# Optimization experiments

Measured on AMD Instinct MI355X. Metric: run time of the kernel, lower is better.

Reference implementation:

```python
import jax, jax.numpy as jnp
import numpy as np

N_NODES = 100000


def _gcn_conv(x, W, b, row, col, norm, n_nodes):
    # PyG GCNConv: h = x @ W; out[i] = sum_{(j->i)} norm_e * h[j] + b
    h = x @ W
    msg = h[row] * norm[:, None]              # [E_tot, out_dim] gather
    out = jax.ops.segment_sum(msg, col, num_segments=n_nodes)  # scatter-add
    return out + b


def _norm_and_loops(edge_index, n_nodes):
    # add self loops, compute symmetric normalization deg^-1/2 * deg^-1/2
    loop = jnp.arange(n_nodes, dtype=edge_index.dtype)
    row = jnp.concatenate([edge_index[0], loop])
    col = jnp.concatenate([edge_index[1], loop])
    deg = jax.ops.segment_sum(jnp.ones_like(col, dtype=jnp.float32), col,
                              num_segments=n_nodes)
    dis = jnp.where(deg > 0, jax.lax.rsqrt(jnp.maximum(deg, 1.0)), 0.0)
    norm = dis[row] * dis[col]
    return row, col, norm


def setup_inputs() -> dict:
    key = jax.random.key(0)
    ks = jax.random.split(key, 9)
    in_c, hid, lat = 128, 128, 64
    n_edges = 1600000
    x = jax.random.normal(ks[0], (N_NODES, in_c), dtype=jnp.float32)
    edge_index = jax.random.randint(ks[1], (2, n_edges), 0, N_NODES, dtype=jnp.int64)
    s1 = 1.0 / np.sqrt(in_c)
    s2 = 1.0 / np.sqrt(hid)
    W1 = jax.random.uniform(ks[2], (in_c, hid), jnp.float32, -s1, s1)
    b1 = jnp.zeros((hid,), jnp.float32)
    W_mu = jax.random.uniform(ks[3], (hid, lat), jnp.float32, -s2, s2)
    b_mu = jnp.zeros((lat,), jnp.float32)
    W_lv = jax.random.uniform(ks[4], (hid, lat), jnp.float32, -s2, s2)
    b_lv = jnp.zeros((lat,), jnp.float32)
    eps = jax.random.normal(ks[5], (N_NODES, lat), dtype=jnp.float32)
    return {"x": x, "edge_index": edge_index, "W1": W1, "b1": b1,
            "W_mu": W_mu, "b_mu": b_mu, "W_lv": W_lv, "b_lv": b_lv,
            "eps": eps}


def reference(x, edge_index, W1, b1, W_mu, b_mu, W_lv, b_lv, eps):
    row, col, norm = _norm_and_loops(edge_index, N_NODES)
    h = jax.nn.relu(_gcn_conv(x, W1, b1, row, col, norm, N_NODES))
    mu = _gcn_conv(h, W_mu, b_mu, row, col, norm, N_NODES)
    logvar = _gcn_conv(h, W_lv, b_lv, row, col, norm, N_NODES)
    # reparameterize (training mode): z = mu + eps * exp(0.5*logvar)
    z = mu + eps * jnp.exp(0.5 * logvar)
    return (z, mu, logvar)
```

## Files before the change

### kernel.cpp

```cpp
#include <hip/hip_runtime.h>
#include <math.h>


#define SHIFT 9
#define EPB 2048
#define BSTRIDE 12288
#define CAP 15104

using f32x4 = __attribute__((ext_vector_type(4))) float;
using f32x2 = __attribute__((ext_vector_type(2))) float;
using f16x8 = __attribute__((ext_vector_type(8))) _Float16;
using f16x2 = __attribute__((ext_vector_type(2))) _Float16;

__device__ inline int scan256(int v, int* wsum) {
    __syncthreads();
    int lane = threadIdx.x & 63, wid = threadIdx.x >> 6;
    int s = v;
#pragma unroll
    for (int d = 1; d < 64; d <<= 1) {
        int u = __shfl_up(s, d, 64);
        if (lane >= d) s += u;
    }
    if (lane == 63) wsum[wid] = s;
    __syncthreads();
    int off = 0;
    for (int w = 0; w < wid; w++) off += wsum[w];
    return off + s - v;
}

__global__ __launch_bounds__(256) void k_bucket(const int* __restrict__ rowi,
                                                const int* __restrict__ coli,
                                                int* __restrict__ bcur,
                                                int* __restrict__ recs,
                                                int E, int NB) {
    __shared__ int lh[4][256], lcur[4][256], excl[256], gbase[256], wsum[4];
    __shared__ int2 stage[EPB];
    int t = threadIdx.x, w = t >> 6;
    lh[0][t] = 0; lh[1][t] = 0; lh[2][t] = 0; lh[3][t] = 0;
    __syncthreads();
    int base = blockIdx.x * EPB;
    int nE = min(EPB, E - base);
    for (int i = t; i < nE; i += 256)
        atomicAdd(&lh[w][coli[base + i] >> SHIFT], 1);
    __syncthreads();
    int h0 = lh[0][t], h1 = lh[1][t], h2 = lh[2][t], h3 = lh[3][t];
    int tot = h0 + h1 + h2 + h3;
    int ex = scan256(tot, wsum);
    excl[t] = ex;
    lcur[0][t] = ex;
    lcur[1][t] = ex + h0;
    lcur[2][t] = ex + h0 + h1;
    lcur[3][t] = ex + h0 + h1 + h2;
    if (t < NB && tot)
        gbase[t] = t * BSTRIDE + atomicAdd(&bcur[t], tot);
    __syncthreads();
    for (int i = t; i < nE; i += 256) {
        int r = rowi[base + i], c = coli[base + i];
        int p = atomicAdd(&lcur[w][c >> SHIFT], 1);
        stage[p] = make_int2(r, c);
    }
    __syncthreads();
    for (int i = t; i < nE; i += 256) {
        int2 r = stage[i];
        int bb = r.y >> SHIFT;
        int idx = gbase[bb] + (i - excl[bb]);
        if (idx - bb * BSTRIDE < BSTRIDE)
            recs[idx] = (r.x << SHIFT) | (r.y & 511);
    }
}

__global__ __launch_bounds__(256) void k_fill2(const int* __restrict__ recs,
                                               const int* __restrict__ bcur,
                                               int2* __restrict__ rowse,
                                               float* __restrict__ dis,
                                               int* __restrict__ srcs, int N) {
    __shared__ int hist[512], excl[512], wsum[4];
    __shared__ int srcsL[CAP];
    int t = threadIdx.x;
    int b = blockIdx.x;
    int nbase = b << SHIFT;
    int start = b * BSTRIDE;
    int cnt = min(bcur[b], BSTRIDE);
    int end = start + cnt;
    hist[t] = 0;
    hist[t + 256] = 0;
    __syncthreads();
    for (int i = start + t; i < end; i += 256)
        atomicAdd(&hist[recs[i] & 511], 1);
    __syncthreads();
    int h0 = hist[2 * t], h1 = hist[2 * t + 1];
    int e0 = scan256(h0 + h1, wsum);
    excl[2 * t] = e0;
    excl[2 * t + 1] = e0 + h0;
    int n0 = nbase + 2 * t, n1 = nbase + 2 * t + 1;
    if (n0 < N) {
        rowse[n0] = make_int2(start + e0, start + e0 + h0);
        dis[n0] = rsqrtf((float)(h0 + 1));
    }
    if (n1 < N) {
        rowse[n1] = make_int2(start + e0 + h0, start + e0 + h0 + h1);
        dis[n1] = rsqrtf((float)(h1 + 1));
    }
    __syncthreads();
    if (cnt <= CAP) {
        for (int i = start + t; i < end; i += 256) {
            int r = recs[i];
            int p = atomicAdd(&excl[r & 511], 1);
            srcsL[p] = ((unsigned)r) >> SHIFT;
        }
        __syncthreads();
        for (int i = t; i < cnt; i += 256) srcs[start + i] = srcsL[i];
    } else {
        for (int i = start + t; i < end; i += 256) {
            int r = recs[i];
            int p = atomicAdd(&excl[r & 511], 1);
            srcs[start + p] = ((unsigned)r) >> SHIFT;
        }
    }
}

template <bool XF16>
__global__ __launch_bounds__(256) void k_gemm(const void* __restrict__ Xv,
                                              const float* __restrict__ Wa,
                                              const float* __restrict__ Wb,
                                              int split,
                                              _Float16* __restrict__ Y,
                                              int M, int ngroups,
                                              int* __restrict__ zcur, int nz) {
    __shared__ _Float16 Wl[16384];
    int tid = threadIdx.x;
    if (zcur && blockIdx.x == 0 && tid < nz) zcur[tid] = 0;
    int wbs = 128 - split;
    for (int i = tid; i < 16384; i += 256) {
        int k = i >> 7, n = i & 127;
        float v = (n < split) ? Wa[k * split + n] : Wb[k * wbs + (n - split)];
        int tt = n >> 4, c = (k >> 5), q = (k >> 3) & 3, ln = q * 16 + (n & 15);
        Wl[(((tt * 4 + c) * 64) + ln) * 8 + (k & 7)] = (_Float16)v;
    }
    __syncthreads();

    int lane = tid & 63, w = tid >> 6;
    f16x8 B[32];
#pragma unroll
    for (int i = 0; i < 32; i++)
        B[i] = *(const f16x8*)&Wl[(i * 64 + lane) * 8];

    int m16 = lane & 15, quad = lane >> 4;
    for (int g = blockIdx.x; g < ngroups; g += gridDim.x) {
        int rowbase = g * 64 + w * 16;
        if (rowbase >= M) continue;
        int arow = min(rowbase + m16, M - 1);
        f16x8 A[4];
        if (XF16) {
            const _Float16* X = (const _Float16*)Xv;
#pragma unroll
            for (int c = 0; c < 4; c++)
                A[c] = *(const f16x8*)&X[arow * 128 + c * 32 + quad * 8];
        } else {
            const float* X = (const float*)Xv;
#pragma unroll
            for (int c = 0; c < 4; c++) {
                float4 u0 = *(const float4*)&X[arow * 128 + c * 32 + quad * 8];
                float4 u1 = *(const float4*)&X[arow * 128 + c * 32 + quad * 8 + 4];
                f16x8 a;
                a[0] = (_Float16)u0.x; a[1] = (_Float16)u0.y;
                a[2] = (_Float16)u0.z; a[3] = (_Float16)u0.w;
                a[4] = (_Float16)u1.x; a[5] = (_Float16)u1.y;
                a[6] = (_Float16)u1.z; a[7] = (_Float16)u1.w;
                A[c] = a;
            }
        }

        f32x4 acc[8];
#pragma unroll
        for (int t = 0; t < 8; t++) acc[t] = (f32x4)(0.f);
#pragma unroll
        for (int t = 0; t < 8; t++)
#pragma unroll
            for (int c = 0; c < 4; c++)
                acc[t] = __builtin_amdgcn_mfma_f32_16x16x32_f16(
                    A[c], B[t * 4 + c], acc[t], 0, 0, 0);

#pragma unroll
        for (int r = 0; r < 4; r++) {
            int row = rowbase + quad * 4 + r;
            if (row < M) {
#pragma unroll
                for (int t = 0; t < 8; t++)
                    Y[row * 128 + t * 16 + m16] = (_Float16)acc[t][r];
            }
        }
    }
}

template <bool OF16>
__global__ __launch_bounds__(256) void k_agg(const _Float16* __restrict__ F,
                                             const float* __restrict__ dis,
                                             const int2* __restrict__ rowse,
                                             const int* __restrict__ srcs,
                                             const float* __restrict__ ba,
                                             const float* __restrict__ bb,
                                             void* __restrict__ outA,
                                             void* __restrict__ outB,
                                             const float* __restrict__ eps,
                                             float* __restrict__ z, int N) {
    int node = blockIdx.x * 4 + (threadIdx.x >> 6);
    if (node >= N) return;
    int lane = threadIdx.x & 63;
    int g = lane >> 4, sl = lane & 15;
    const f16x8* Fr = (const f16x8*)F;

    float di = dis[node];
    float acc[8];
#pragma unroll
    for (int j = 0; j < 8; j++) acc[j] = 0.f;
    if (g == 0) {
        f16x8 v = Fr[node * 16 + sl];
#pragma unroll
        for (int j = 0; j < 8; j++) acc[j] = di * (float)v[j];
    }

    int2 se = rowse[node];
    int s = se.x, e = se.y;
    int t = s;
    for (; t + 16 <= e; t += 16) {
        int i0 = srcs[t + g];
        int i1 = srcs[t + 4 + g];
        int i2 = srcs[t + 8 + g];
        int i3 = srcs[t + 12 + g];
        float d0 = dis[i0], d1 = dis[i1], d2 = dis[i2], d3 = dis[i3];
        f16x8 v0 = Fr[i0 * 16 + sl];
        f16x8 v1 = Fr[i1 * 16 + sl];
        f16x8 v2 = Fr[i2 * 16 + sl];
        f16x8 v3 = Fr[i3 * 16 + sl];
#pragma unroll
        for (int j = 0; j < 8; j++)
            acc[j] = fmaf(d0, (float)v0[j],
                     fmaf(d1, (float)v1[j],
                     fmaf(d2, (float)v2[j],
                     fmaf(d3, (float)v3[j], acc[j]))));
    }
    if (t + 8 <= e) {
        int i0 = srcs[t + g];
        int i1 = srcs[t + 4 + g];
        float d0 = dis[i0], d1 = dis[i1];
        f16x8 v0 = Fr[i0 * 16 + sl];
        f16x8 v1 = Fr[i1 * 16 + sl];
#pragma unroll
        for (int j = 0; j < 8; j++)
            acc[j] = fmaf(d0, (float)v0[j], fmaf(d1, (float)v1[j], acc[j]));
        t += 8;
    }
    if (t + 4 <= e) {
        int i0 = srcs[t + g];
        float d0 = dis[i0];
        f16x8 v0 = Fr[i0 * 16 + sl];
#pragma unroll
        for (int j = 0; j < 8; j++) acc[j] = fmaf(d0, (float)v0[j], acc[j]);
        t += 4;
    }
    if (t < e) {
        int idx = t + g;
        bool ok = idx < e;
        int i0 = ok ? srcs[idx] : 0;
        float d0 = dis[i0];
        f16x8 v0 = Fr[i0 * 16 + sl];
        if (ok) {
#pragma unroll
            for (int j = 0; j < 8; j++) acc[j] = fmaf(d0, (float)v0[j], acc[j]);
        }
    }

#pragma unroll
    for (int j = 0; j < 8; j++) {
        acc[j] += __shfl_xor(acc[j], 16);
        acc[j] += __shfl_xor(acc[j], 32);
    }

    if constexpr (OF16) {
        float4 b0 = *(const float4*)&ba[sl * 8];
        float4 b1 = *(const float4*)&ba[sl * 8 + 4];
        if (lane < 16) {
            f16x8 o;
            o[0] = (_Float16)fmaxf(fmaf(di, acc[0], b0.x), 0.f);
            o[1] = (_Float16)fmaxf(fmaf(di, acc[1], b0.y), 0.f);
            o[2] = (_Float16)fmaxf(fmaf(di, acc[2], b0.z), 0.f);
            o[3] = (_Float16)fmaxf(fmaf(di, acc[3], b0.w), 0.f);
            o[4] = (_Float16)fmaxf(fmaf(di, acc[4], b1.x), 0.f);
            o[5] = (_Float16)fmaxf(fmaf(di, acc[5], b1.y), 0.f);
            o[6] = (_Float16)fmaxf(fmaf(di, acc[6], b1.z), 0.f);
            o[7] = (_Float16)fmaxf(fmaf(di, acc[7], b1.w), 0.f);
            ((f16x8*)outA)[node * 16 + sl] = o;
        }
    } else {
        const float* bp = (sl < 8) ? ba : bb;
        int cb = (sl & 7) * 8;
        float4 b0 = *(const float4*)&bp[cb];
        float4 b1 = *(const float4*)&bp[cb + 4];
        float o[8];
        o[0] = fmaf(di, acc[0], b0.x);
        o[1] = fmaf(di, acc[1], b0.y);
        o[2] = fmaf(di, acc[2], b0.z);
        o[3] = fmaf(di, acc[3], b0.w);
        o[4] = fmaf(di, acc[4], b1.x);
        o[5] = fmaf(di, acc[5], b1.y);
        o[6] = fmaf(di, acc[6], b1.z);
        o[7] = fmaf(di, acc[7], b1.w);
        if (lane < 16) {
            float* op = (sl < 8) ? (float*)outA : (float*)outB;
            f32x4 s0, s1;
            s0[0] = o[0]; s0[1] = o[1]; s0[2] = o[2]; s0[3] = o[3];
            s1[0] = o[4]; s1[1] = o[5]; s1[2] = o[6]; s1[3] = o[7];
            __builtin_nontemporal_store(s0, (f32x4*)&op[node * 64 + cb]);
            __builtin_nontemporal_store(s1, (f32x4*)&op[node * 64 + cb + 4]);
        }
        float lvv[8];
#pragma unroll
        for (int j = 0; j < 8; j++) lvv[j] = __shfl_xor(o[j], 8);
        if (lane < 8) {
            int zb = node * 64 + sl * 8;
            float4 e0 = *(const float4*)&eps[zb];
            float4 e1 = *(const float4*)&eps[zb + 4];
            f32x4 z0, z1;
            z0[0] = fmaf(e0.x, expf(0.5f * lvv[0]), o[0]);
            z0[1] = fmaf(e0.y, expf(0.5f * lvv[1]), o[1]);
            z0[2] = fmaf(e0.z, expf(0.5f * lvv[2]), o[2]);
            z0[3] = fmaf(e0.w, expf(0.5f * lvv[3]), o[3]);
            z1[0] = fmaf(e1.x, expf(0.5f * lvv[4]), o[4]);
            z1[1] = fmaf(e1.y, expf(0.5f * lvv[5]), o[5]);
            z1[2] = fmaf(e1.z, expf(0.5f * lvv[6]), o[6]);
            z1[3] = fmaf(e1.w, expf(0.5f * lvv[7]), o[7]);
            __builtin_nontemporal_store(z0, (f32x4*)&z[zb]);
            __builtin_nontemporal_store(z1, (f32x4*)&z[zb + 4]);
        }
    }
}

extern "C" void kernel_launch(void* const* d_in, const int* in_sizes, int n_in,
                              void* d_out, int out_size, void* d_ws, size_t ws_size,
                              hipStream_t stream) {
    const float* x   = (const float*)d_in[0];
    const int*   ei  = (const int*)d_in[1];
    const float* W1  = (const float*)d_in[2];
    const float* b1  = (const float*)d_in[3];
    const float* Wmu = (const float*)d_in[4];
    const float* bmu = (const float*)d_in[5];
    const float* Wlv = (const float*)d_in[6];
    const float* blv = (const float*)d_in[7];
    const float* eps = (const float*)d_in[8];

    int N = in_sizes[0] / 128;
    int E = in_sizes[1] / 2;
    const int* rowi = ei;
    const int* coli = ei + E;
    int NB = (N + (1 << SHIFT) - 1) >> SHIFT;

    char* ws = (char*)d_ws;
    size_t off = 0;
    auto alloc = [&](size_t bytes) -> void* {
        void* p = ws + off;
        off += (bytes + 255) & ~(size_t)255;
        return p;
    };
    _Float16* bufA = (_Float16*)alloc((size_t)N * 128 * 2);
    _Float16* bufB = (_Float16*)alloc((size_t)N * 128 * 2);
    float* dis    = (float*)alloc((size_t)N * 4);
    int2*  rowse  = (int2*)alloc((size_t)N * 8);
    int*   srcs   = (int*)alloc((size_t)NB * BSTRIDE * 4);
    int*   recs   = (int*)alloc((size_t)NB * BSTRIDE * 4);
    int*   bcur   = (int*)alloc((size_t)NB * 4);

    float* zo  = (float*)d_out;
    float* muo = zo + (size_t)N * 64;
    float* lvo = zo + (size_t)N * 128;

    int ngroups = (N + 63) / 64;
    int gblk = ngroups < 640 ? ngroups : 640;
    k_gemm<false><<<gblk, 256, 0, stream>>>(x, W1, W1, 128, bufA, N, ngroups,
                                            bcur, NB);
    k_bucket<<<(E + EPB - 1) / EPB, 256, 0, stream>>>(rowi, coli, bcur, recs,
                                                      E, NB);
    k_fill2<<<NB, 256, 0, stream>>>(recs, bcur, rowse, dis, srcs, N);
    k_agg<true><<<(N + 3) / 4, 256, 0, stream>>>(bufA, dis, rowse, srcs,
                                                 b1, b1, bufB, bufB,
                                                 nullptr, nullptr, N);
    k_gemm<true><<<gblk, 256, 0, stream>>>(bufB, Wmu, Wlv, 64, bufA, N, ngroups,
                                           nullptr, 0);
    k_agg<false><<<(N + 3) / 4, 256, 0, stream>>>(bufA, dis, rowse, srcs,
                                                  bmu, blv, muo, lvo,
                                                  eps, zo, N);
}
```

Before: 381.5 us.

## Partition feature matrix into 16-column planes for cache-local aggregation

The GEMM now writes its fp16 output as eight column planes of 16 halves per node, and the second GEMM reads its input in the matching permuted plane layout. The aggregation kernel gives each block a single plane, so all blocks working on one plane gather from a 3.2 MB slice that fits in cache, instead of every gather touching full 256-byte rows. Each wave handles 32 nodes and processes 16 edges at a time with 4-lane groups, then reduces across lanes with shuffles. In exchange, the source index, dis and rowse arrays are read eight times, and each gather loads only 8 bytes per lane.

```diff
diff --git a/kernel.cpp b/kernel.cpp
--- a/kernel.cpp
+++ b/kernel.cpp
@@ -6,10 +6,12 @@
 #define EPB 2048
 #define BSTRIDE 12288
 #define CAP 15104
+#define WNODES 32
 
 using f32x4 = __attribute__((ext_vector_type(4))) float;
 using f32x2 = __attribute__((ext_vector_type(2))) float;
 using f16x8 = __attribute__((ext_vector_type(8))) _Float16;
+using f16x4 = __attribute__((ext_vector_type(4))) _Float16;
 using f16x2 = __attribute__((ext_vector_type(2))) _Float16;
 
 __device__ inline int scan256(int v, int* wsum) {
@@ -119,7 +121,7 @@
     }
 }
 
-template <bool XF16>
+template <bool L2>
 __global__ __launch_bounds__(256) void k_gemm(const void* __restrict__ Xv,
                                               const float* __restrict__ Wa,
                                               const float* __restrict__ Wb,
@@ -146,16 +148,19 @@
         B[i] = *(const f16x8*)&Wl[(i * 64 + lane) * 8];
 
     int m16 = lane & 15, quad = lane >> 4;
+    int M16 = M * 16;
     for (int g = blockIdx.x; g < ngroups; g += gridDim.x) {
         int rowbase = g * 64 + w * 16;
         if (rowbase >= M) continue;
         int arow = min(rowbase + m16, M - 1);
         f16x8 A[4];
-        if (XF16) {
+        if (L2) {
             const _Float16* X = (const _Float16*)Xv;
 #pragma unroll
-            for (int c = 0; c < 4; c++)
-                A[c] = *(const f16x8*)&X[arow * 128 + c * 32 + quad * 8];
+            for (int c = 0; c < 4; c++) {
+                int pa = 2 * c + (quad >> 1);
+                A[c] = *(const f16x8*)&X[pa * M16 + arow * 16 + (quad & 1) * 8];
+            }
         } else {
             const float* X = (const float*)Xv;
 #pragma unroll
@@ -186,8 +191,16 @@
             int row = rowbase + quad * 4 + r;
             if (row < M) {
 #pragma unroll
-                for (int t = 0; t < 8; t++)
-                    Y[row * 128 + t * 16 + m16] = (_Float16)acc[t][r];
+                for (int t = 0; t < 8; t++) {
+                    if (!L2) {
+                        Y[t * M16 + row * 16 + m16] = (_Float16)acc[t][r];
+                    } else {
+                        int p = (t < 4) ? (2 * t + (m16 >> 3))
+                                        : (2 * (t - 4) + (m16 >> 3));
+                        int slot = ((t < 4) ? 0 : 8) + (m16 & 7);
+                        Y[p * M16 + row * 16 + slot] = (_Float16)acc[t][r];
+                    }
+                }
             }
         }
     }
@@ -204,134 +217,82 @@
                                              void* __restrict__ outB,
                                              const float* __restrict__ eps,
                                              float* __restrict__ z, int N) {
-    int node = blockIdx.x * 4 + (threadIdx.x >> 6);
-    if (node >= N) return;
-    int lane = threadIdx.x & 63;
-    int g = lane >> 4, sl = lane & 15;
-    const f16x8* Fr = (const f16x8*)F;
-
-    float di = dis[node];
-    float acc[8];
-#pragma unroll
-    for (int j = 0; j < 8; j++) acc[j] = 0.f;
-    if (g == 0) {
-        f16x8 v = Fr[node * 16 + sl];
-#pragma unroll
-        for (int j = 0; j < 8; j++) acc[j] = di * (float)v[j];
-    }
-
-    int2 se = rowse[node];
-    int s = se.x, e = se.y;
-    int t = s;
-    for (; t + 16 <= e; t += 16) {
-        int i0 = srcs[t + g];
-        int i1 = srcs[t + 4 + g];
-        int i2 = srcs[t + 8 + g];
-        int i3 = srcs[t + 12 + g];
-        float d0 = dis[i0], d1 = dis[i1], d2 = dis[i2], d3 = dis[i3];
-        f16x8 v0 = Fr[i0 * 16 + sl];
-        f16x8 v1 = Fr[i1 * 16 + sl];
-        f16x8 v2 = Fr[i2 * 16 + sl];
-        f16x8 v3 = Fr[i3 * 16 + sl];
-#pragma unroll
-        for (int j = 0; j < 8; j++)
-            acc[j] = fmaf(d0, (float)v0[j],
-                     fmaf(d1, (float)v1[j],
-                     fmaf(d2, (float)v2[j],
-                     fmaf(d3, (float)v3[j], acc[j]))));
-    }
-    if (t + 8 <= e) {
-        int i0 = srcs[t + g];
-        int i1 = srcs[t + 4 + g];
-        float d0 = dis[i0], d1 = dis[i1];
-        f16x8 v0 = Fr[i0 * 16 + sl];
-        f16x8 v1 = Fr[i1 * 16 + sl];
-#pragma unroll
-        for (int j = 0; j < 8; j++)
-            acc[j] = fmaf(d0, (float)v0[j], fmaf(d1, (float)v1[j], acc[j]));
-        t += 8;
-    }
-    if (t + 4 <= e) {
-        int i0 = srcs[t + g];
-        float d0 = dis[i0];
-        f16x8 v0 = Fr[i0 * 16 + sl];
-#pragma unroll
-        for (int j = 0; j < 8; j++) acc[j] = fmaf(d0, (float)v0[j], acc[j]);
-        t += 4;
-    }
-    if (t < e) {
-        int idx = t + g;
-        bool ok = idx < e;
-        int i0 = ok ? srcs[idx] : 0;
-        float d0 = dis[i0];
-        f16x8 v0 = Fr[i0 * 16 + sl];
-        if (ok) {
-#pragma unroll
-            for (int j = 0; j < 8; j++) acc[j] = fmaf(d0, (float)v0[j], acc[j]);
-        }
-    }
-
-#pragma unroll
-    for (int j = 0; j < 8; j++) {
-        acc[j] += __shfl_xor(acc[j], 16);
-        acc[j] += __shfl_xor(acc[j], 32);
-    }
-
-    if constexpr (OF16) {
-        float4 b0 = *(const float4*)&ba[sl * 8];
-        float4 b1 = *(const float4*)&ba[sl * 8 + 4];
-        if (lane < 16) {
-            f16x8 o;
-            o[0] = (_Float16)fmaxf(fmaf(di, acc[0], b0.x), 0.f);
-            o[1] = (_Float16)fmaxf(fmaf(di, acc[1], b0.y), 0.f);
-            o[2] = (_Float16)fmaxf(fmaf(di, acc[2], b0.z), 0.f);
-            o[3] = (_Float16)fmaxf(fmaf(di, acc[3], b0.w), 0.f);
-            o[4] = (_Float16)fmaxf(fmaf(di, acc[4], b1.x), 0.f);
-            o[5] = (_Float16)fmaxf(fmaf(di, acc[5], b1.y), 0.f);
-            o[6] = (_Float16)fmaxf(fmaf(di, acc[6], b1.z), 0.f);
-            o[7] = (_Float16)fmaxf(fmaf(di, acc[7], b1.w), 0.f);
-            ((f16x8*)outA)[node * 16 + sl] = o;
-        }
-    } else {
-        const float* bp = (sl < 8) ? ba : bb;
-        int cb = (sl & 7) * 8;
-        float4 b0 = *(const float4*)&bp[cb];
-        float4 b1 = *(const float4*)&bp[cb + 4];
-        float o[8];
-        o[0] = fmaf(di, acc[0], b0.x);
-        o[1] = fmaf(di, acc[1], b0.y);
-        o[2] = fmaf(di, acc[2], b0.z);
-        o[3] = fmaf(di, acc[3], b0.w);
-        o[4] = fmaf(di, acc[4], b1.x);
-        o[5] = fmaf(di, acc[5], b1.y);
-        o[6] = fmaf(di, acc[6], b1.z);
-        o[7] = fmaf(di, acc[7], b1.w);
-        if (lane < 16) {
-            float* op = (sl < 8) ? (float*)outA : (float*)outB;
-            f32x4 s0, s1;
-            s0[0] = o[0]; s0[1] = o[1]; s0[2] = o[2]; s0[3] = o[3];
-            s1[0] = o[4]; s1[1] = o[5]; s1[2] = o[6]; s1[3] = o[7];
-            __builtin_nontemporal_store(s0, (f32x4*)&op[node * 64 + cb]);
-            __builtin_nontemporal_store(s1, (f32x4*)&op[node * 64 + cb + 4]);
-        }
-        float lvv[8];
-#pragma unroll
-        for (int j = 0; j < 8; j++) lvv[j] = __shfl_xor(o[j], 8);
-        if (lane < 8) {
-            int zb = node * 64 + sl * 8;
-            float4 e0 = *(const float4*)&eps[zb];
-            float4 e1 = *(const float4*)&eps[zb + 4];
-            f32x4 z0, z1;
-            z0[0] = fmaf(e0.x, expf(0.5f * lvv[0]), o[0]);
-            z0[1] = fmaf(e0.y, expf(0.5f * lvv[1]), o[1]);
-            z0[2] = fmaf(e0.z, expf(0.5f * lvv[2]), o[2]);
-            z0[3] = fmaf(e0.w, expf(0.5f * lvv[3]), o[3]);
-            z1[0] = fmaf(e1.x, expf(0.5f * lvv[4]), o[4]);
-            z1[1] = fmaf(e1.y, expf(0.5f * lvv[5]), o[5]);
-            z1[2] = fmaf(e1.z, expf(0.5f * lvv[6]), o[6]);
-            z1[3] = fmaf(e1.w, expf(0.5f * lvv[7]), o[7]);
-            __builtin_nontemporal_store(z0, (f32x4*)&z[zb]);
-            __builtin_nontemporal_store(z1, (f32x4*)&z[zb + 4]);
+    int p = blockIdx.x & 7;
+    int chunk = blockIdx.x >> 3;
+    int wid = threadIdx.x >> 6, lane = threadIdx.x & 63;
+    int esub = lane >> 2, sq = lane & 3;
+    int N16 = N * 16;
+    const _Float16* Fp = F + p * N16;
+
+    int nodebase = (chunk * 4 + wid) * WNODES;
+    for (int ni = 0; ni < WNODES; ni++) {
+        int node = nodebase + ni;
+        if (node >= N) return;
+        int2 se = rowse[node];
+        float di = dis[node];
+        float a0 = 0.f, a1 = 0.f, a2 = 0.f, a3 = 0.f;
+        for (int t = se.x; t < se.y; t += 16) {
+            int eidx = t + esub;
+            bool ok = eidx < se.y;
+            int src = ok ? __builtin_nontemporal_load(&srcs[eidx]) : 0;
+            float d = ok ? dis[src] : 0.f;
+            f16x4 v = *(const f16x4*)&Fp[src * 16 + sq * 4];
+            a0 = fmaf(d, (float)v[0], a0);
+            a1 = fmaf(d, (float)v[1], a1);
+            a2 = fmaf(d, (float)v[2], a2);
+            a3 = fmaf(d, (float)v[3], a3);
+        }
+#pragma unroll
+        for (int m = 4; m <= 32; m <<= 1) {
+            a0 += __shfl_xor(a0, m);
+            a1 += __shfl_xor(a1, m);
+            a2 += __shfl_xor(a2, m);
+            a3 += __shfl_xor(a3, m);
+        }
+        f16x4 vs = *(const f16x4*)&Fp[node * 16 + sq * 4];
+        a0 = fmaf(di, (float)vs[0], a0);
+        a1 = fmaf(di, (float)vs[1], a1);
+        a2 = fmaf(di, (float)vs[2], a2);
+        a3 = fmaf(di, (float)vs[3], a3);
+
+        if constexpr (OF16) {
+            if (lane < 4) {
+                float4 b = *(const float4*)&ba[p * 16 + sq * 4];
+                f16x4 o;
+                o[0] = (_Float16)fmaxf(fmaf(di, a0, b.x), 0.f);
+                o[1] = (_Float16)fmaxf(fmaf(di, a1, b.y), 0.f);
+                o[2] = (_Float16)fmaxf(fmaf(di, a2, b.z), 0.f);
+                o[3] = (_Float16)fmaxf(fmaf(di, a3, b.w), 0.f);
+                *(f16x4*)&((_Float16*)outA)[p * N16 + node * 16 + sq * 4] = o;
+            }
+        } else {
+            bool isMu = sq < 2;
+            int cb = p * 8 + (sq & 1) * 4;
+            const float* bp = isMu ? ba : bb;
+            float4 b = *(const float4*)&bp[cb];
+            float o0 = fmaf(di, a0, b.x);
+            float o1 = fmaf(di, a1, b.y);
+            float o2 = fmaf(di, a2, b.z);
+            float o3 = fmaf(di, a3, b.w);
+            if (lane < 4) {
+                float* op = isMu ? (float*)outA : (float*)outB;
+                f32x4 s;
+                s[0] = o0; s[1] = o1; s[2] = o2; s[3] = o3;
+                __builtin_nontemporal_store(s, (f32x4*)&op[node * 64 + cb]);
+            }
+            float l0 = __shfl_xor(o0, 2);
+            float l1 = __shfl_xor(o1, 2);
+            float l2 = __shfl_xor(o2, 2);
+            float l3 = __shfl_xor(o3, 2);
+            if (lane < 2) {
+                float4 e = *(const float4*)&eps[node * 64 + cb];
+                f32x4 zv;
+                zv[0] = fmaf(e.x, expf(0.5f * l0), o0);
+                zv[1] = fmaf(e.y, expf(0.5f * l1), o1);
+                zv[2] = fmaf(e.z, expf(0.5f * l2), o2);
+                zv[3] = fmaf(e.w, expf(0.5f * l3), o3);
+                __builtin_nontemporal_store(zv, (f32x4*)&z[node * 64 + cb]);
+            }
         }
     }
 }
@@ -376,17 +337,18 @@
 
     int ngroups = (N + 63) / 64;
     int gblk = ngroups < 640 ? ngroups : 640;
+    int aggblk = ((N + 127) / 128) * 8;
     k_gemm<false><<<gblk, 256, 0, stream>>>(x, W1, W1, 128, bufA, N, ngroups,
                                             bcur, NB);
     k_bucket<<<(E + EPB - 1) / EPB, 256, 0, stream>>>(rowi, coli, bcur, recs,
                                                       E, NB);
     k_fill2<<<NB, 256, 0, stream>>>(recs, bcur, rowse, dis, srcs, N);
-    k_agg<true><<<(N + 3) / 4, 256, 0, stream>>>(bufA, dis, rowse, srcs,
-                                                 b1, b1, bufB, bufB,
-                                                 nullptr, nullptr, N);
+    k_agg<true><<<aggblk, 256, 0, stream>>>(bufA, dis, rowse, srcs,
+                                            b1, b1, bufB, bufB,
+                                            nullptr, nullptr, N);
     k_gemm<true><<<gblk, 256, 0, stream>>>(bufB, Wmu, Wlv, 64, bufA, N, ngroups,
                                            nullptr, 0);
-    k_agg<false><<<(N + 3) / 4, 256, 0, stream>>>(bufA, dis, rowse, srcs,
-                                                  bmu, blv, muo, lvo,
-                                                  eps, zo, N);
-}
+    k_agg<false><<<aggblk, 256, 0, stream>>>(bufA, dis, rowse, srcs,
+                                             bmu, blv, muo, lvo,
+                                             eps, zo, N);
+}
```

New measurement: 1.012 ms. 2.65x slower.

## Fuse first GEMM, edge bucketing and CSR fill into one persistent kernel

Applied to the files above, without the earlier changes.

Merges the first layer GEMM, the edge bucketing pass and the per-bucket CSR fill into a single persistent kernel of 512 blocks. The phases are separated by a software grid barrier built on atomics and a generation counter. The goal is to remove two kernel launches and their tail gaps, which matter when the whole pipeline runs in a few hundred microseconds. In exchange, the fill phase always stages sources in shared memory with no fallback when a bucket overflows, the barrier depends on all 512 blocks being co-resident, and fewer blocks are available for the bucketing and GEMM phases.

```diff
diff --git a/kernel.cpp b/kernel.cpp
--- a/kernel.cpp
+++ b/kernel.cpp
@@ -5,12 +5,10 @@
 #define SHIFT 9
 #define EPB 2048
 #define BSTRIDE 12288
-#define CAP 15104
+#define NBLD 512
 
 using f32x4 = __attribute__((ext_vector_type(4))) float;
-using f32x2 = __attribute__((ext_vector_type(2))) float;
 using f16x8 = __attribute__((ext_vector_type(8))) _Float16;
-using f16x2 = __attribute__((ext_vector_type(2))) _Float16;
 
 __device__ inline int scan256(int v, int* wsum) {
     __syncthreads();
@@ -28,108 +26,185 @@
     return off + s - v;
 }
 
-__global__ __launch_bounds__(256) void k_bucket(const int* __restrict__ rowi,
-                                                const int* __restrict__ coli,
-                                                int* __restrict__ bcur,
-                                                int* __restrict__ recs,
-                                                int E, int NB) {
-    __shared__ int lh[4][256], lcur[4][256], excl[256], gbase[256], wsum[4];
-    __shared__ int2 stage[EPB];
+__device__ inline void gridbar(int* bar, int nblk) {
+    __syncthreads();
+    if (threadIdx.x == 0) {
+        __threadfence();
+        int gen = __hip_atomic_load(&bar[1], __ATOMIC_ACQUIRE,
+                                    __HIP_MEMORY_SCOPE_AGENT);
+        int v = atomicAdd(&bar[0], 1);
+        if (v == nblk - 1) {
+            bar[0] = 0;
+            __threadfence();
+            atomicAdd(&bar[1], 1);
+        } else {
+            while (__hip_atomic_load(&bar[1], __ATOMIC_ACQUIRE,
+                                     __HIP_MEMORY_SCOPE_AGENT) == gen)
+                __builtin_amdgcn_s_sleep(8);
+        }
+    }
+    __syncthreads();
+}
+
+__global__ __launch_bounds__(256, 2) void k_build(
+        const float* __restrict__ x, const float* __restrict__ W1,
+        _Float16* __restrict__ Y, int M, int ngroups,
+        const int* __restrict__ rowi, const int* __restrict__ coli,
+        int* __restrict__ bcur, int* __restrict__ recs, int E, int nchunks,
+        int2* __restrict__ rowse, float* __restrict__ dis,
+        int* __restrict__ srcs, int NB, int* __restrict__ bar) {
+    __shared__ __align__(16) char smem[53264];
     int t = threadIdx.x, w = t >> 6;
-    lh[0][t] = 0; lh[1][t] = 0; lh[2][t] = 0; lh[3][t] = 0;
-    __syncthreads();
-    int base = blockIdx.x * EPB;
-    int nE = min(EPB, E - base);
-    for (int i = t; i < nE; i += 256)
-        atomicAdd(&lh[w][coli[base + i] >> SHIFT], 1);
-    __syncthreads();
-    int h0 = lh[0][t], h1 = lh[1][t], h2 = lh[2][t], h3 = lh[3][t];
-    int tot = h0 + h1 + h2 + h3;
-    int ex = scan256(tot, wsum);
-    excl[t] = ex;
-    lcur[0][t] = ex;
-    lcur[1][t] = ex + h0;
-    lcur[2][t] = ex + h0 + h1;
-    lcur[3][t] = ex + h0 + h1 + h2;
-    if (t < NB && tot)
-        gbase[t] = t * BSTRIDE + atomicAdd(&bcur[t], tot);
-    __syncthreads();
-    for (int i = t; i < nE; i += 256) {
-        int r = rowi[base + i], c = coli[base + i];
-        int p = atomicAdd(&lcur[w][c >> SHIFT], 1);
-        stage[p] = make_int2(r, c);
-    }
-    __syncthreads();
-    for (int i = t; i < nE; i += 256) {
-        int2 r = stage[i];
-        int bb = r.y >> SHIFT;
-        int idx = gbase[bb] + (i - excl[bb]);
-        if (idx - bb * BSTRIDE < BSTRIDE)
-            recs[idx] = (r.x << SHIFT) | (r.y & 511);
-    }
-}
-
-__global__ __launch_bounds__(256) void k_fill2(const int* __restrict__ recs,
-                                               const int* __restrict__ bcur,
-                                               int2* __restrict__ rowse,
-                                               float* __restrict__ dis,
-                                               int* __restrict__ srcs, int N) {
-    __shared__ int hist[512], excl[512], wsum[4];
-    __shared__ int srcsL[CAP];
-    int t = threadIdx.x;
-    int b = blockIdx.x;
-    int nbase = b << SHIFT;
-    int start = b * BSTRIDE;
-    int cnt = min(bcur[b], BSTRIDE);
-    int end = start + cnt;
-    hist[t] = 0;
-    hist[t + 256] = 0;
-    __syncthreads();
-    for (int i = start + t; i < end; i += 256)
-        atomicAdd(&hist[recs[i] & 511], 1);
-    __syncthreads();
-    int h0 = hist[2 * t], h1 = hist[2 * t + 1];
-    int e0 = scan256(h0 + h1, wsum);
-    excl[2 * t] = e0;
-    excl[2 * t + 1] = e0 + h0;
-    int n0 = nbase + 2 * t, n1 = nbase + 2 * t + 1;
-    if (n0 < N) {
-        rowse[n0] = make_int2(start + e0, start + e0 + h0);
-        dis[n0] = rsqrtf((float)(h0 + 1));
-    }
-    if (n1 < N) {
-        rowse[n1] = make_int2(start + e0 + h0, start + e0 + h0 + h1);
-        dis[n1] = rsqrtf((float)(h1 + 1));
-    }
-    __syncthreads();
-    if (cnt <= CAP) {
-        for (int i = start + t; i < end; i += 256) {
-            int r = recs[i];
-            int p = atomicAdd(&excl[r & 511], 1);
-            srcsL[p] = ((unsigned)r) >> SHIFT;
+
+    if (blockIdx.x == 0 && t < NB) bcur[t] = 0;
+    {
+        _Float16* Wl = (_Float16*)smem;
+        for (int i = t; i < 16384; i += 256) {
+            int k = i >> 7, n = i & 127;
+            float v = W1[k * 128 + n];
+            int tt = n >> 4, c = (k >> 5), q = (k >> 3) & 3,
+                ln = q * 16 + (n & 15);
+            Wl[(((tt * 4 + c) * 64) + ln) * 8 + (k & 7)] = (_Float16)v;
         }
         __syncthreads();
-        for (int i = t; i < cnt; i += 256) srcs[start + i] = srcsL[i];
-    } else {
-        for (int i = start + t; i < end; i += 256) {
-            int r = recs[i];
-            int p = atomicAdd(&excl[r & 511], 1);
-            srcs[start + p] = ((unsigned)r) >> SHIFT;
-        }
-    }
-}
-
-template <bool XF16>
-__global__ __launch_bounds__(256) void k_gemm(const void* __restrict__ Xv,
-                                              const float* __restrict__ Wa,
-                                              const float* __restrict__ Wb,
-                                              int split,
-                                              _Float16* __restrict__ Y,
-                                              int M, int ngroups,
-                                              int* __restrict__ zcur, int nz) {
+        int lane = t & 63;
+        f16x8 B[32];
+#pragma unroll
+        for (int i = 0; i < 32; i++)
+            B[i] = *(const f16x8*)&Wl[(i * 64 + lane) * 8];
+        int m16 = lane & 15, quad = lane >> 4;
+        for (int g = blockIdx.x; g < ngroups; g += gridDim.x) {
+            int rowbase = g * 64 + w * 16;
+            if (rowbase >= M) continue;
+            int arow = min(rowbase + m16, M - 1);
+            f16x8 A[4];
+#pragma unroll
+            for (int c = 0; c < 4; c++) {
+                float4 u0 = *(const float4*)&x[arow * 128 + c * 32 + quad * 8];
+                float4 u1 = *(const float4*)&x[arow * 128 + c * 32 + quad * 8 + 4];
+                f16x8 a;
+                a[0] = (_Float16)u0.x; a[1] = (_Float16)u0.y;
+                a[2] = (_Float16)u0.z; a[3] = (_Float16)u0.w;
+                a[4] = (_Float16)u1.x; a[5] = (_Float16)u1.y;
+                a[6] = (_Float16)u1.z; a[7] = (_Float16)u1.w;
+                A[c] = a;
+            }
+            f32x4 acc[8];
+#pragma unroll
+            for (int tt = 0; tt < 8; tt++) acc[tt] = (f32x4)(0.f);
+#pragma unroll
+            for (int tt = 0; tt < 8; tt++)
+#pragma unroll
+                for (int c = 0; c < 4; c++)
+                    acc[tt] = __builtin_amdgcn_mfma_f32_16x16x32_f16(
+                        A[c], B[tt * 4 + c], acc[tt], 0, 0, 0);
+#pragma unroll
+            for (int r = 0; r < 4; r++) {
+                int row = rowbase + quad * 4 + r;
+                if (row < M) {
+#pragma unroll
+                    for (int tt = 0; tt < 8; tt++)
+                        Y[row * 128 + tt * 16 + m16] = (_Float16)acc[tt][r];
+                }
+            }
+        }
+    }
+    gridbar(bar, NBLD);
+
+    {
+        int* lh    = (int*)smem;
+        int* lcur  = lh + 1024;
+        int* bexcl = lcur + 1024;
+        int* gbase = bexcl + 256;
+        int* bwsum = gbase + 256;
+        int2* stage = (int2*)(bwsum + 4);
+        for (int chunk = blockIdx.x; chunk < nchunks; chunk += gridDim.x) {
+            __syncthreads();
+            lh[t] = 0; lh[256 + t] = 0; lh[512 + t] = 0; lh[768 + t] = 0;
+            __syncthreads();
+            int base = chunk * EPB;
+            int nE = min(EPB, E - base);
+            for (int i = t; i < nE; i += 256)
+                atomicAdd(&lh[w * 256 + (coli[base + i] >> SHIFT)], 1);
+            __syncthreads();
+            int h0 = lh[t], h1 = lh[256 + t], h2 = lh[512 + t], h3 = lh[768 + t];
+            int tot = h0 + h1 + h2 + h3;
+            int ex = scan256(tot, bwsum);
+            bexcl[t] = ex;
+            lcur[t] = ex;
+            lcur[256 + t] = ex + h0;
+            lcur[512 + t] = ex + h0 + h1;
+            lcur[768 + t] = ex + h0 + h1 + h2;
+            if (t < NB && tot)
+                gbase[t] = t * BSTRIDE + atomicAdd(&bcur[t], tot);
+            __syncthreads();
+            for (int i = t; i < nE; i += 256) {
+                int r = rowi[base + i], c = coli[base + i];
+                int p = atomicAdd(&lcur[w * 256 + (c >> SHIFT)], 1);
+                stage[p] = make_int2(r, c);
+            }
+            __syncthreads();
+            for (int i = t; i < nE; i += 256) {
+                int2 r = stage[i];
+                int bb = r.y >> SHIFT;
+                int idx = gbase[bb] + (i - bexcl[bb]);
+                if (idx - bb * BSTRIDE < BSTRIDE)
+                    recs[idx] = (r.x << SHIFT) | (r.y & 511);
+            }
+        }
+    }
+    gridbar(bar, NBLD);
+
+    {
+        int* hist  = (int*)smem;
+        int* fexcl = hist + 512;
+        int* fwsum = fexcl + 512;
+        int* srcsL = fwsum + 4;
+        for (int b = blockIdx.x; b < NB; b += gridDim.x) {
+            __syncthreads();
+            int nbase = b << SHIFT;
+            int start = b * BSTRIDE;
+            int cnt = min(bcur[b], BSTRIDE);
+            int end = start + cnt;
+            hist[t] = 0;
+            hist[t + 256] = 0;
+            __syncthreads();
+            for (int i = start + t; i < end; i += 256)
+                atomicAdd(&hist[recs[i] & 511], 1);
+            __syncthreads();
+            int h0 = hist[2 * t], h1 = hist[2 * t + 1];
+            int e0 = scan256(h0 + h1, fwsum);
+            fexcl[2 * t] = e0;
+            fexcl[2 * t + 1] = e0 + h0;
+            int n0 = nbase + 2 * t, n1 = nbase + 2 * t + 1;
+            if (n0 < M) {
+                rowse[n0] = make_int2(start + e0, start + e0 + h0);
+                dis[n0] = rsqrtf((float)(h0 + 1));
+            }
+            if (n1 < M) {
+                rowse[n1] = make_int2(start + e0 + h0, start + e0 + h0 + h1);
+                dis[n1] = rsqrtf((float)(h1 + 1));
+            }
+            __syncthreads();
+            for (int i = start + t; i < end; i += 256) {
+                int r = recs[i];
+                int p = atomicAdd(&fexcl[r & 511], 1);
+                srcsL[p] = ((unsigned)r) >> SHIFT;
+            }
+            __syncthreads();
+            for (int i = t; i < cnt; i += 256) srcs[start + i] = srcsL[i];
+        }
+    }
+}
+
+__global__ __launch_bounds__(256) void k_gemm2(const _Float16* __restrict__ X,
+                                               const float* __restrict__ Wa,
+                                               const float* __restrict__ Wb,
+                                               int split,
+                                               _Float16* __restrict__ Y,
+                                               int M, int ngroups) {
     __shared__ _Float16 Wl[16384];
     int tid = threadIdx.x;
-    if (zcur && blockIdx.x == 0 && tid < nz) zcur[tid] = 0;
     int wbs = 128 - split;
     for (int i = tid; i < 16384; i += 256) {
         int k = i >> 7, n = i & 127;
@@ -151,25 +226,9 @@
         if (rowbase >= M) continue;
         int arow = min(rowbase + m16, M - 1);
         f16x8 A[4];
-        if (XF16) {
-            const _Float16* X = (const _Float16*)Xv;
-#pragma unroll
-            for (int c = 0; c < 4; c++)
-                A[c] = *(const f16x8*)&X[arow * 128 + c * 32 + quad * 8];
-        } else {
-            const float* X = (const float*)Xv;
-#pragma unroll
-            for (int c = 0; c < 4; c++) {
-                float4 u0 = *(const float4*)&X[arow * 128 + c * 32 + quad * 8];
-                float4 u1 = *(const float4*)&X[arow * 128 + c * 32 + quad * 8 + 4];
-                f16x8 a;
-                a[0] = (_Float16)u0.x; a[1] = (_Float16)u0.y;
-                a[2] = (_Float16)u0.z; a[3] = (_Float16)u0.w;
-                a[4] = (_Float16)u1.x; a[5] = (_Float16)u1.y;
-                a[6] = (_Float16)u1.z; a[7] = (_Float16)u1.w;
-                A[c] = a;
-            }
-        }
+#pragma unroll
+        for (int c = 0; c < 4; c++)
+            A[c] = *(const f16x8*)&X[arow * 128 + c * 32 + quad * 8];
 
         f32x4 acc[8];
 #pragma unroll
@@ -354,6 +413,7 @@
     const int* rowi = ei;
     const int* coli = ei + E;
     int NB = (N + (1 << SHIFT) - 1) >> SHIFT;
+    int nchunks = (E + EPB - 1) / EPB;
 
     char* ws = (char*)d_ws;
     size_t off = 0;
@@ -369,23 +429,23 @@
     int*   srcs   = (int*)alloc((size_t)NB * BSTRIDE * 4);
     int*   recs   = (int*)alloc((size_t)NB * BSTRIDE * 4);
     int*   bcur   = (int*)alloc((size_t)NB * 4);
+    int*   bar    = (int*)alloc(8);
 
     float* zo  = (float*)d_out;
     float* muo = zo + (size_t)N * 64;
     float* lvo = zo + (size_t)N * 128;
 
     int ngroups = (N + 63) / 64;
-    int gblk = ngroups < 640 ? ngroups : 640;
-    k_gemm<false><<<gblk, 256, 0, stream>>>(x, W1, W1, 128, bufA, N, ngroups,
-                                            bcur, NB);
-    k_bucket<<<(E + EPB - 1) / EPB, 256, 0, stream>>>(rowi, coli, bcur, recs,
-                                                      E, NB);
-    k_fill2<<<NB, 256, 0, stream>>>(recs, bcur, rowse, dis, srcs, N);
+
+    hipMemsetAsync(bar, 0, 8, stream);
+    k_build<<<NBLD, 256, 0, stream>>>(x, W1, bufA, N, ngroups, rowi, coli,
+                                      bcur, recs, E, nchunks, rowse, dis,
+                                      srcs, NB, bar);
     k_agg<true><<<(N + 3) / 4, 256, 0, stream>>>(bufA, dis, rowse, srcs,
                                                  b1, b1, bufB, bufB,
                                                  nullptr, nullptr, N);
-    k_gemm<true><<<gblk, 256, 0, stream>>>(bufB, Wmu, Wlv, 64, bufA, N, ngroups,
-                                           nullptr, 0);
+    int gblk = ngroups < 640 ? ngroups : 640;
+    k_gemm2<<<gblk, 256, 0, stream>>>(bufB, Wmu, Wlv, 64, bufA, N, ngroups);
     k_agg<false><<<(N + 3) / 4, 256, 0, stream>>>(bufA, dis, rowse, srcs,
                                                   bmu, blv, muo, lvo,
                                                   eps, zo, N);
```

New measurement: 543.1 us. +42.4%, slower.
